# Kernel tuning notes

Hardware: AMD Instinct MI355X
Metric: run time of the kernel (lower is better)

The kernel has to match this reference:

```python
import jax, jax.numpy as jnp
import numpy as np

COL = 14
NJ = 14
SIGMA = 1.0
RADIUS = int(4.0 * SIGMA + 0.5)  # scipy gaussian_filter default truncate=4.0 -> radius 4

def _gaussian_matrix():
    # 1D operator matrix G[y_out, y_src] of scipy.ndimage.gaussian_filter with
    # sigma=1, mode='reflect' (== numpy 'symmetric' padding) on a length-COL axis.
    w = np.exp(-0.5 * (np.arange(-RADIUS, RADIUS + 1) / SIGMA) ** 2)
    w = w / w.sum()
    eye_p = np.pad(np.eye(COL), ((RADIUS, RADIUS), (0, 0)), mode='symmetric')
    G = sum(w[k] * eye_p[k:k + COL] for k in range(2 * RADIUS + 1))
    return jnp.asarray(G.astype(np.float32))

G_MAT = _gaussian_matrix()

def setup_inputs():
    key = jax.random.key(0)
    k1, k2, k3 = jax.random.split(key, 3)
    B = 8192
    out = jax.random.normal(k1, (B, 3 * NJ, COL, COL), dtype=jnp.float32)
    t = jax.random.uniform(k2, (B, NJ, 2), dtype=jnp.float32)  # normalized coords in [0,1)
    v = jax.random.randint(k3, (B, NJ, 1), 0, 2).astype(jnp.float32)
    v = jnp.tile(v, (1, 1, 2))  # visibility flag duplicated over (x,y) channels
    return {"out": out, "t": t, "v": v}

def _forward(out, t, v):
    B = out.shape[0]
    scale = 1.0 / COL
    h = out[:, :NJ]          # [B,NJ,COL,COL] heatmaps
    o = out[:, NJ:]          # [B,2*NJ,COL,COL] offset maps (x offsets then y offsets)
    # per-joint argmax over flattened grid (first-occurrence, same as torch .max)
    idx = jnp.argmax(h.reshape(B, NJ, COL * COL), axis=-1)    # [B,NJ]
    yc = idx // COL
    xc = idx % COL
    # gather offsets at the argmax location
    o_flat = o.reshape(B, 2 * NJ, COL * COL)
    ox = jnp.take_along_axis(o_flat[:, :NJ], idx[:, :, None], axis=2)[..., 0]
    oy = jnp.take_along_axis(o_flat[:, NJ:], idx[:, :, None], axis=2)[..., 0]
    x_pred = jnp.stack([(ox + xc.astype(out.dtype)) * scale,
                        (oy + yc.astype(out.dtype)) * scale], axis=-1)  # [B,NJ,2]
    # gaussian target construction (constant w.r.t. the network output)
    ti = (t * COL).astype(jnp.int32)      # int() truncation; t >= 0
    xi, yi = ti[..., 0], ti[..., 1]
    inb = (xi >= 0) & (xi <= COL - 1) & (yi >= 0) & (yi <= COL - 1)
    vis = v[..., 0].astype(jnp.int32) == 1
    scat = vis & inb                       # joints that receive a gaussian target
    v_eff = jnp.where((vis & ~inb)[..., None], 0.0, v)  # out-of-bounds visible -> zeroed
    # gaussian-filtered one-hot == outer(G[:,yi], G[:,xi]) (separable splat)
    gy = G_MAT.T[jnp.clip(yi, 0, COL - 1)]   # [B,NJ,COL]
    gx = G_MAT.T[jnp.clip(xi, 0, COL - 1)]   # [B,NJ,COL]
    tt = gy[..., :, None] * gx[..., None, :]  # [B,NJ,COL,COL]
    mn = tt.min(axis=(2, 3), keepdims=True)
    mx = tt.max(axis=(2, 3), keepdims=True)
    tt = jnp.where(scat[..., None, None], (tt - mn) / (mx - mn), 0.0)
    # heatmap loss; original zeroes only ROW 0 of the map for invisible joints
    diff1 = h - tt
    vis_eff = (v_eff[..., 0].astype(jnp.int32) == 1)
    diff1 = diff1.at[:, :, 0, :].set(diff1[:, :, 0, :] * vis_eff[..., None].astype(diff1.dtype))
    cnt = jnp.sum(vis_eff.astype(jnp.float32))
    d1 = jnp.sum(diff1 * diff1) / cnt
    # coordinate loss, masked by (possibly updated) visibility
    diff2 = (x_pred - t) * v_eff
    n2 = v_eff.sum() / 2.0
    d2 = jnp.sum(diff2 * diff2) / n2
    return d1 + d2

def reference(out, t, v):
    return _forward(out, t, v)
```

## Files before the change

### kernel.cpp

```cpp
#include <hip/hip_runtime.h>


#define COL 14
#define NJ 14
#define CELLS (COL * COL)
#define THREADS 256
#define WPB (THREADS / 64)
#define BLOCKS 2048
#define MAXI 16
#define NEGINF -3.402823466e38f

__global__ __launch_bounds__(THREADS)
void mse3_main(const float* __restrict__ outp, const float* __restrict__ tp,
               const float* __restrict__ vp, double* __restrict__ partial, int npair)
{
    __shared__ float Gs[CELLS];
    __shared__ float cminS[COL], cmaxS[COL];
    __shared__ double part[WPB][4];

    const int tid = threadIdx.x;

    if (tid < CELLS) {
        const double wraw[9] = {3.3546262790251185e-4, 1.1108996538242306e-2,
                                1.353352832366127e-1,  6.065306597126334e-1, 1.0,
                                6.065306597126334e-1,  1.353352832366127e-1,
                                1.1108996538242306e-2, 3.3546262790251185e-4};
        const double Z = 2.5066208042307818;
        int gi = tid / COL;
        int gj = tid - COL * gi;
        double a = 0.0;
#pragma unroll
        for (int k = 0; k < 9; ++k) {
            int r = gi + k;
            int m = (r < 4) ? (3 - r) : ((r < 18) ? (r - 4) : (31 - r));
            if (m == gj) a += wraw[k] / Z;
        }
        Gs[tid] = (float)a;
    }
    __syncthreads();
    if (tid < COL) {
        float mn = Gs[tid], mx = mn;
        for (int r = 1; r < COL; ++r) {
            float g = Gs[r * COL + tid];
            mn = fminf(mn, g);
            mx = fmaxf(mx, g);
        }
        cminS[tid] = mn;
        cmaxS[tid] = mx;
    }
    __syncthreads();

    const int lane   = tid & 63;
    const int wv     = tid >> 6;
    const int gwave  = blockIdx.x * WPB + wv;
    const int nwaves = BLOCKS * WPB;

    float s1 = 0.0f, s2 = 0.0f, cnt = 0.0f, n2 = 0.0f;

    for (int pbase = gwave; pbase < npair; pbase += nwaves * MAXI) {
        const int m = min(MAXI, (npair - pbase + nwaves - 1) / nwaves);

        int packreg = 0;
        float tvx = 0.f, tvy = 0.f, vvx = 0.f, vvy = 0.f;
        if (lane < m) {
            int p = pbase + lane * nwaves;
            float2 tv = reinterpret_cast<const float2*>(tp)[p];
            float2 vv = reinterpret_cast<const float2*>(vp)[p];
            tvx = tv.x; tvy = tv.y; vvx = vv.x; vvy = vv.y;
            int xi = (int)(tv.x * 14.0f);
            int yi = (int)(tv.y * 14.0f);
            bool inb    = (xi >= 0) && (xi <= COL - 1) && (yi >= 0) && (yi <= COL - 1);
            bool vis    = ((int)vv.x == 1);
            bool scat   = vis && inb;
            bool zeroed = vis && !inb;
            float ve0   = zeroed ? 0.0f : vv.x;
            bool vise   = ((int)ve0 == 1);
            int xic = min(max(xi, 0), COL - 1);
            int yic = min(max(yi, 0), COL - 1);
            packreg = xic | (yic << 4) | (scat ? 256 : 0) | (vise ? 512 : 0)
                          | (zeroed ? 1024 : 0);
        }

        float4 hv_next = make_float4(0.f, 0.f, 0.f, 0.f);
        if (lane < 49) {
            int b = pbase / NJ, j = pbase - NJ * b;
            hv_next = reinterpret_cast<const float4*>(
                outp + ((size_t)b * (3 * NJ) + j) * CELLS)[lane];
        }

        int myidx = 0;
        for (int i = 0; i < m; ++i) {
            float4 hv = hv_next;
            if (i + 1 < m && lane < 49) {
                int p = pbase + (i + 1) * nwaves;
                int b = p / NJ, j = p - NJ * b;
                hv_next = reinterpret_cast<const float4*>(
                    outp + ((size_t)b * (3 * NJ) + j) * CELLS)[lane];
            }
            const int pk = __shfl(packreg, i, 64);
            const int xic = pk & 15;
            const int yic = (pk >> 4) & 15;
            const bool scat = (pk & 256) != 0;
            const bool vise = (pk & 512) != 0;

            float best = NEGINF;
            int bidx = 0;
            if (lane < 49) {
                best = hv.x; bidx = 4 * lane;
                if (hv.y > best) { best = hv.y; bidx = 4 * lane + 1; }
                if (hv.z > best) { best = hv.z; bidx = 4 * lane + 2; }
                if (hv.w > best) { best = hv.w; bidx = 4 * lane + 3; }
            }
#pragma unroll
            for (int off = 32; off >= 1; off >>= 1) {
                float ov = __shfl_down(best, off, 64);
                int   oi = __shfl_down(bidx, off, 64);
                if (ov > best || (ov == best && oi < bidx)) { best = ov; bidx = oi; }
            }
            const int idxb = __shfl(bidx, 0, 64);
            if (lane == i) myidx = idxb;

            if (lane < 49) {
                float h4[4] = {hv.x, hv.y, hv.z, hv.w};
                int y = (4 * lane) / COL;
                int x = 4 * lane - COL * y;
                if (scat) {
                    float mn  = cminS[yic] * cminS[xic];
                    float mx  = cmaxS[yic] * cmaxS[xic];
                    float inv = 1.0f / (mx - mn);
#pragma unroll
                    for (int c = 0; c < 4; ++c) {
                        float tt = (Gs[y * COL + yic] * Gs[x * COL + xic] - mn) * inv;
                        float d = h4[c] - tt;
                        if (y == 0 && !vise) d = 0.0f;
                        s1 += d * d;
                        ++x; if (x == COL) { x = 0; ++y; }
                    }
                } else {
#pragma unroll
                    for (int c = 0; c < 4; ++c) {
                        float d = h4[c];
                        if (y == 0 && !vise) d = 0.0f;
                        s1 += d * d;
                        ++x; if (x == COL) { x = 0; ++y; }
                    }
                }
            }
        }

        if (lane < m) {
            int p = pbase + lane * nwaves;
            int b = p / NJ, j = p - NJ * b;
            const float* base = outp + (size_t)b * (3 * NJ) * CELLS;
            float ox = base[(size_t)(NJ + j) * CELLS + myidx];
            float oy = base[(size_t)(2 * NJ + j) * CELLS + myidx];
            bool zeroed = (packreg & 1024) != 0;
            bool vise   = (packreg & 512) != 0;
            float ve0 = zeroed ? 0.0f : vvx;
            float ve1 = zeroed ? 0.0f : vvy;
            int yc = myidx / COL;
            int xc = myidx - COL * yc;
            const float SC = (float)(1.0 / 14.0);
            float dx = (ox + (float)xc) * SC - tvx; dx *= ve0;
            float dy = (oy + (float)yc) * SC - tvy; dy *= ve1;
            s2 += dx * dx + dy * dy;
            if (vise) cnt += 1.0f;
            n2 += ve0 + ve1;
        }
    }

#pragma unroll
    for (int off = 32; off >= 1; off >>= 1) {
        s1  += __shfl_down(s1,  off, 64);
        s2  += __shfl_down(s2,  off, 64);
        cnt += __shfl_down(cnt, off, 64);
        n2  += __shfl_down(n2,  off, 64);
    }
    if (lane == 0) {
        part[wv][0] = (double)s1;
        part[wv][1] = (double)s2;
        part[wv][2] = (double)cnt;
        part[wv][3] = (double)n2;
    }
    __syncthreads();
    if (tid == 0) {
        double a0 = 0, a1 = 0, a2 = 0, a3 = 0;
        for (int i = 0; i < WPB; ++i) {
            a0 += part[i][0]; a1 += part[i][1];
            a2 += part[i][2]; a3 += part[i][3];
        }
        double* o = partial + (size_t)blockIdx.x * 4;
        o[0] = a0; o[1] = a1; o[2] = a2; o[3] = a3;
    }
}

__global__ __launch_bounds__(256)
void mse3_final(const double* __restrict__ partial, float* __restrict__ o)
{
    __shared__ double p2[4][4];
    double a0 = 0, a1 = 0, a2 = 0, a3 = 0;
    for (int b = threadIdx.x; b < BLOCKS; b += 256) {
        const double* q = partial + (size_t)b * 4;
        a0 += q[0]; a1 += q[1]; a2 += q[2]; a3 += q[3];
    }
#pragma unroll
    for (int off = 32; off >= 1; off >>= 1) {
        a0 += __shfl_down(a0, off, 64);
        a1 += __shfl_down(a1, off, 64);
        a2 += __shfl_down(a2, off, 64);
        a3 += __shfl_down(a3, off, 64);
    }
    const int lane = threadIdx.x & 63, wv = threadIdx.x >> 6;
    if (lane == 0) { p2[wv][0] = a0; p2[wv][1] = a1; p2[wv][2] = a2; p2[wv][3] = a3; }
    __syncthreads();
    if (threadIdx.x == 0) {
        double s1 = 0, s2 = 0, cn = 0, nn = 0;
        for (int i = 0; i < 4; ++i) {
            s1 += p2[i][0]; s2 += p2[i][1]; cn += p2[i][2]; nn += p2[i][3];
        }
        o[0] = (float)(s1 / cn + s2 / (0.5 * nn));
    }
}

extern "C" void kernel_launch(void* const* d_in, const int* in_sizes, int n_in,
                              void* d_out, int out_size, void* d_ws, size_t ws_size,
                              hipStream_t stream)
{
    const float* outp = (const float*)d_in[0];
    const float* tp   = (const float*)d_in[1];
    const float* vp   = (const float*)d_in[2];
    double* partial = (double*)d_ws;

    const int B = in_sizes[0] / (3 * NJ * CELLS);
    const int npair = B * NJ;

    mse3_main<<<BLOCKS, THREADS, 0, stream>>>(outp, tp, vp, partial, npair);
    mse3_final<<<1, 256, 0, stream>>>(partial, (float*)d_out);
}
```

Before: 331.8 us.

## Switch from wave-per-joint to thread-per-joint processing with register prefetch

```diff
diff --git a/kernel.cpp b/kernel.cpp
--- a/kernel.cpp
+++ b/kernel.cpp
@@ -4,30 +4,27 @@
 #define COL 14
 #define NJ 14
 #define CELLS (COL * COL)
-#define THREADS 256
-#define WPB (THREADS / 64)
-#define BLOCKS 2048
-#define MAXI 16
+#define TPB 64
+#define PFD 8
 #define NEGINF -3.402823466e38f
 
-__global__ __launch_bounds__(THREADS)
+__global__ __launch_bounds__(TPB)
 void mse3_main(const float* __restrict__ outp, const float* __restrict__ tp,
                const float* __restrict__ vp, double* __restrict__ partial, int npair)
 {
     __shared__ float Gs[CELLS];
     __shared__ float cminS[COL], cmaxS[COL];
-    __shared__ double part[WPB][4];
 
     const int tid = threadIdx.x;
 
-    if (tid < CELLS) {
+    for (int g = tid; g < CELLS; g += TPB) {
         const double wraw[9] = {3.3546262790251185e-4, 1.1108996538242306e-2,
                                 1.353352832366127e-1,  6.065306597126334e-1, 1.0,
                                 6.065306597126334e-1,  1.353352832366127e-1,
                                 1.1108996538242306e-2, 3.3546262790251185e-4};
         const double Z = 2.5066208042307818;
-        int gi = tid / COL;
-        int gj = tid - COL * gi;
+        int gi = g / COL;
+        int gj = g - COL * gi;
         double a = 0.0;
 #pragma unroll
         for (int k = 0; k < 9; ++k) {
@@ -35,7 +32,7 @@
             int m = (r < 4) ? (3 - r) : ((r < 18) ? (r - 4) : (31 - r));
             if (m == gj) a += wraw[k] / Z;
         }
-        Gs[tid] = (float)a;
+        Gs[g] = (float)a;
     }
     __syncthreads();
     if (tid < COL) {
@@ -50,123 +47,79 @@
     }
     __syncthreads();
 
-    const int lane   = tid & 63;
-    const int wv     = tid >> 6;
-    const int gwave  = blockIdx.x * WPB + wv;
-    const int nwaves = BLOCKS * WPB;
+    const int p = blockIdx.x * TPB + tid;
 
     float s1 = 0.0f, s2 = 0.0f, cnt = 0.0f, n2 = 0.0f;
 
-    for (int pbase = gwave; pbase < npair; pbase += nwaves * MAXI) {
-        const int m = min(MAXI, (npair - pbase + nwaves - 1) / nwaves);
+    if (p < npair) {
+        const int b = p / NJ;
+        const int j = p - NJ * b;
+        const float4* hp4 = reinterpret_cast<const float4*>(
+            outp + ((size_t)b * (3 * NJ) + j) * CELLS);
 
-        int packreg = 0;
-        float tvx = 0.f, tvy = 0.f, vvx = 0.f, vvy = 0.f;
-        if (lane < m) {
-            int p = pbase + lane * nwaves;
-            float2 tv = reinterpret_cast<const float2*>(tp)[p];
-            float2 vv = reinterpret_cast<const float2*>(vp)[p];
-            tvx = tv.x; tvy = tv.y; vvx = vv.x; vvy = vv.y;
-            int xi = (int)(tv.x * 14.0f);
-            int yi = (int)(tv.y * 14.0f);
-            bool inb    = (xi >= 0) && (xi <= COL - 1) && (yi >= 0) && (yi <= COL - 1);
-            bool vis    = ((int)vv.x == 1);
-            bool scat   = vis && inb;
-            bool zeroed = vis && !inb;
-            float ve0   = zeroed ? 0.0f : vv.x;
-            bool vise   = ((int)ve0 == 1);
-            int xic = min(max(xi, 0), COL - 1);
-            int yic = min(max(yi, 0), COL - 1);
-            packreg = xic | (yic << 4) | (scat ? 256 : 0) | (vise ? 512 : 0)
-                          | (zeroed ? 1024 : 0);
-        }
+        const float2 tv = reinterpret_cast<const float2*>(tp)[p];
+        const float2 vv = reinterpret_cast<const float2*>(vp)[p];
+        const int xi = (int)(tv.x * 14.0f);
+        const int yi = (int)(tv.y * 14.0f);
+        const bool inb    = (xi >= 0) && (xi <= COL - 1) && (yi >= 0) && (yi <= COL - 1);
+        const bool vis    = ((int)vv.x == 1);
+        const bool scat   = vis && inb;
+        const bool zeroed = vis && !inb;
+        const float ve0   = zeroed ? 0.0f : vv.x;
+        const float ve1   = zeroed ? 0.0f : vv.y;
+        const bool vise   = ((int)ve0 == 1);
+        const float vm    = vise ? 1.0f : 0.0f;
+        const int xic = min(max(xi, 0), COL - 1);
+        const int yic = min(max(yi, 0), COL - 1);
 
-        float4 hv_next = make_float4(0.f, 0.f, 0.f, 0.f);
-        if (lane < 49) {
-            int b = pbase / NJ, j = pbase - NJ * b;
-            hv_next = reinterpret_cast<const float4*>(
-                outp + ((size_t)b * (3 * NJ) + j) * CELLS)[lane];
-        }
+        const float mnv = cminS[yic] * cminS[xic];
+        const float mxv = cmaxS[yic] * cmaxS[xic];
+        const float A      = scat ? (1.0f / (mxv - mnv)) : 0.0f;
+        const float mnAneg = -mnv * A;
 
-        int myidx = 0;
-        for (int i = 0; i < m; ++i) {
-            float4 hv = hv_next;
-            if (i + 1 < m && lane < 49) {
-                int p = pbase + (i + 1) * nwaves;
-                int b = p / NJ, j = p - NJ * b;
-                hv_next = reinterpret_cast<const float4*>(
-                    outp + ((size_t)b * (3 * NJ) + j) * CELLS)[lane];
-            }
-            const int pk = __shfl(packreg, i, 64);
-            const int xic = pk & 15;
-            const int yic = (pk >> 4) & 15;
-            const bool scat = (pk & 256) != 0;
-            const bool vise = (pk & 512) != 0;
+        float gyv[COL], gxA[COL];
+#pragma unroll
+        for (int y = 0; y < COL; ++y) gyv[y] = Gs[y * COL + yic];
+#pragma unroll
+        for (int x = 0; x < COL; ++x) gxA[x] = Gs[x * COL + xic] * A;
 
-            float best = NEGINF;
-            int bidx = 0;
-            if (lane < 49) {
-                best = hv.x; bidx = 4 * lane;
-                if (hv.y > best) { best = hv.y; bidx = 4 * lane + 1; }
-                if (hv.z > best) { best = hv.z; bidx = 4 * lane + 2; }
-                if (hv.w > best) { best = hv.w; bidx = 4 * lane + 3; }
-            }
+        float best = NEGINF;
+        int bidx = 0;
+
+        float4 buf[PFD];
 #pragma unroll
-            for (int off = 32; off >= 1; off >>= 1) {
-                float ov = __shfl_down(best, off, 64);
-                int   oi = __shfl_down(bidx, off, 64);
-                if (ov > best || (ov == best && oi < bidx)) { best = ov; bidx = oi; }
-            }
-            const int idxb = __shfl(bidx, 0, 64);
-            if (lane == i) myidx = idxb;
+        for (int d = 0; d < PFD; ++d) buf[d] = hp4[d];
 
-            if (lane < 49) {
-                float h4[4] = {hv.x, hv.y, hv.z, hv.w};
-                int y = (4 * lane) / COL;
-                int x = 4 * lane - COL * y;
-                if (scat) {
-                    float mn  = cminS[yic] * cminS[xic];
-                    float mx  = cmaxS[yic] * cmaxS[xic];
-                    float inv = 1.0f / (mx - mn);
 #pragma unroll
-                    for (int c = 0; c < 4; ++c) {
-                        float tt = (Gs[y * COL + yic] * Gs[x * COL + xic] - mn) * inv;
-                        float d = h4[c] - tt;
-                        if (y == 0 && !vise) d = 0.0f;
-                        s1 += d * d;
-                        ++x; if (x == COL) { x = 0; ++y; }
-                    }
-                } else {
+        for (int c = 0; c < 49; ++c) {
+            float4 hv = buf[c & (PFD - 1)];
+            if (c + PFD < 49) buf[c & (PFD - 1)] = hp4[c + PFD];
+            const float h4[4] = {hv.x, hv.y, hv.z, hv.w};
 #pragma unroll
-                    for (int c = 0; c < 4; ++c) {
-                        float d = h4[c];
-                        if (y == 0 && !vise) d = 0.0f;
-                        s1 += d * d;
-                        ++x; if (x == COL) { x = 0; ++y; }
-                    }
-                }
+            for (int q = 0; q < 4; ++q) {
+                const int e = 4 * c + q;
+                const int y = e / COL;
+                const int x = e - COL * y;
+                const float h = h4[q];
+                if (h > best) { best = h; bidx = e; }
+                float ttv = fmaf(gyv[y], gxA[x], mnAneg);
+                float d1 = h - ttv;
+                if (e < COL) d1 *= vm;
+                s1 = fmaf(d1, d1, s1);
             }
         }
 
-        if (lane < m) {
-            int p = pbase + lane * nwaves;
-            int b = p / NJ, j = p - NJ * b;
-            const float* base = outp + (size_t)b * (3 * NJ) * CELLS;
-            float ox = base[(size_t)(NJ + j) * CELLS + myidx];
-            float oy = base[(size_t)(2 * NJ + j) * CELLS + myidx];
-            bool zeroed = (packreg & 1024) != 0;
-            bool vise   = (packreg & 512) != 0;
-            float ve0 = zeroed ? 0.0f : vvx;
-            float ve1 = zeroed ? 0.0f : vvy;
-            int yc = myidx / COL;
-            int xc = myidx - COL * yc;
-            const float SC = (float)(1.0 / 14.0);
-            float dx = (ox + (float)xc) * SC - tvx; dx *= ve0;
-            float dy = (oy + (float)yc) * SC - tvy; dy *= ve1;
-            s2 += dx * dx + dy * dy;
-            if (vise) cnt += 1.0f;
-            n2 += ve0 + ve1;
-        }
+        const float* base = outp + (size_t)b * (3 * NJ) * CELLS;
+        const float ox = base[(size_t)(NJ + j) * CELLS + bidx];
+        const float oy = base[(size_t)(2 * NJ + j) * CELLS + bidx];
+        const int yc = bidx / COL;
+        const int xc = bidx - COL * yc;
+        const float SC = (float)(1.0 / 14.0);
+        float dx = (ox + (float)xc) * SC - tv.x; dx *= ve0;
+        float dy = (oy + (float)yc) * SC - tv.y; dy *= ve1;
+        s2  = dx * dx + dy * dy;
+        cnt = vise ? 1.0f : 0.0f;
+        n2  = ve0 + ve1;
     }
 
 #pragma unroll
@@ -176,30 +129,19 @@
         cnt += __shfl_down(cnt, off, 64);
         n2  += __shfl_down(n2,  off, 64);
     }
-    if (lane == 0) {
-        part[wv][0] = (double)s1;
-        part[wv][1] = (double)s2;
-        part[wv][2] = (double)cnt;
-        part[wv][3] = (double)n2;
-    }
-    __syncthreads();
     if (tid == 0) {
-        double a0 = 0, a1 = 0, a2 = 0, a3 = 0;
-        for (int i = 0; i < WPB; ++i) {
-            a0 += part[i][0]; a1 += part[i][1];
-            a2 += part[i][2]; a3 += part[i][3];
-        }
         double* o = partial + (size_t)blockIdx.x * 4;
-        o[0] = a0; o[1] = a1; o[2] = a2; o[3] = a3;
+        o[0] = (double)s1; o[1] = (double)s2;
+        o[2] = (double)cnt; o[3] = (double)n2;
     }
 }
 
 __global__ __launch_bounds__(256)
-void mse3_final(const double* __restrict__ partial, float* __restrict__ o)
+void mse3_final(const double* __restrict__ partial, float* __restrict__ o, int nblk)
 {
     __shared__ double p2[4][4];
     double a0 = 0, a1 = 0, a2 = 0, a3 = 0;
-    for (int b = threadIdx.x; b < BLOCKS; b += 256) {
+    for (int b = threadIdx.x; b < nblk; b += 256) {
         const double* q = partial + (size_t)b * 4;
         a0 += q[0]; a1 += q[1]; a2 += q[2]; a3 += q[3];
     }
@@ -233,7 +175,8 @@
 
     const int B = in_sizes[0] / (3 * NJ * CELLS);
     const int npair = B * NJ;
+    const int nblk = (npair + TPB - 1) / TPB;
 
-    mse3_main<<<BLOCKS, THREADS, 0, stream>>>(outp, tp, vp, partial, npair);
-    mse3_final<<<1, 256, 0, stream>>>(partial, (float*)d_out);
+    mse3_main<<<nblk, TPB, 0, stream>>>(outp, tp, vp, partial, npair);
+    mse3_final<<<1, 256, 0, stream>>>(partial, (float*)d_out, nblk);
 }
```

New measurement: 341.9 us. +3.0%, slower.
